# Kernel tuning notes

Hardware: AMD Instinct MI355X
Metric: run time of the kernel (lower is better)

Reference implementation:

```python
import jax, jax.numpy as jnp
import numpy as np

G = 32               # sdf grid resolution (grid_size init default)
SCALE_FACTOR = 0.2   # forward default scale_factor
EPS = 1e-12


def setup_inputs() -> dict:
    key = jax.random.key(0)
    k1, k2 = jax.random.split(key)
    H, V, F = 2, 778, 1538  # two hands, MANO topology
    vertices = jax.random.normal(k1, (H, V, 3), dtype=jnp.float32)
    faces = jax.random.randint(k2, (F, 3), 0, V, dtype=jnp.int32)
    return {"vertices": vertices, "faces": faces}


def _sdiv(n, d):
    return n / jnp.where(jnp.abs(d) < EPS, EPS, d)


def _point_tri_dist2(p, a, b, c):
    # p: [P,1,3]; a,b,c: [1,F,3] -> squared distance [P,F] (Ericson closest-point)
    ab = b - a; ac = c - a; ap = p - a
    d1 = jnp.sum(ab * ap, -1); d2 = jnp.sum(ac * ap, -1)
    bp = p - b; d3 = jnp.sum(ab * bp, -1); d4 = jnp.sum(ac * bp, -1)
    cp = p - c; d5 = jnp.sum(ab * cp, -1); d6 = jnp.sum(ac * cp, -1)
    vc = d1 * d4 - d3 * d2
    vb = d5 * d2 - d1 * d6
    va = d3 * d6 - d5 * d4
    denom = va + vb + vc
    v_in = _sdiv(vb, denom); w_in = _sdiv(vc, denom)
    res = a + ab * v_in[..., None] + ac * w_in[..., None]  # face interior
    # edge BC
    cond = ((va <= 0) & ((d4 - d3) >= 0) & ((d5 - d6) >= 0))[..., None]
    w = _sdiv(d4 - d3, (d4 - d3) + (d5 - d6))[..., None]
    res = jnp.where(cond, b + (c - b) * w, res)
    # edge AC
    cond = ((vb <= 0) & (d2 >= 0) & (d6 <= 0))[..., None]
    w = _sdiv(d2, d2 - d6)[..., None]
    res = jnp.where(cond, a + ac * w, res)
    # edge AB
    cond = ((vc <= 0) & (d1 >= 0) & (d3 <= 0))[..., None]
    w = _sdiv(d1, d1 - d3)[..., None]
    res = jnp.where(cond, a + ab * w, res)
    # vertex regions (highest precedence)
    res = jnp.where(((d6 >= 0) & (d5 <= d6))[..., None], jnp.broadcast_to(c, res.shape), res)
    res = jnp.where(((d3 >= 0) & (d4 <= d3))[..., None], jnp.broadcast_to(b, res.shape), res)
    res = jnp.where(((d1 <= 0) & (d2 <= 0))[..., None], jnp.broadcast_to(a, res.shape), res)
    return jnp.sum((p - res) ** 2, -1)


def _inside(p, a, b, c):
    # parity of +x ray intersections (Moller-Trumbore with dir = (1,0,0))
    e1 = b - a; e2 = c - a
    det = e1[..., 1] * (-e2[..., 2]) + e1[..., 2] * e2[..., 1]  # dot(e1, cross(dir,e2))
    inv = _sdiv(1.0, det)
    s = p - a
    u = (s[..., 1] * (-e2[..., 2]) + s[..., 2] * e2[..., 1]) * inv
    q = jnp.cross(s, e1)
    v = q[..., 0] * inv                # dot(dir, q)
    t = jnp.sum(e2 * q, -1) * inv
    hit = (jnp.abs(det) > 1e-9) & (u >= 0) & (u <= 1) & (v >= 0) & (u + v <= 1) & (t > 0)
    return (jnp.sum(hit.astype(jnp.int32), axis=-1) % 2) == 1


def _sdf_grid(tri):
    # tri: [F,3,3] scaled triangles -> phi [G,G,G] laid out [z,y,x] (grid_sample DHW)
    a = tri[None, :, 0]; b = tri[None, :, 1]; c = tri[None, :, 2]
    lin = jnp.linspace(-1.0, 1.0, G, dtype=tri.dtype)
    zz, yy, xx = jnp.meshgrid(lin, lin, lin, indexing='ij')
    pts = jnp.stack([xx, yy, zz], -1).reshape(G, G * G, 3)  # chunk over z-slabs

    def slab(ps):
        p = ps[:, None, :]
        d2 = jnp.min(_point_tri_dist2(p, a, b, c), axis=1)
        ins = _inside(p, a, b, c)
        return jnp.where(ins, jnp.sqrt(jnp.maximum(d2, 0.0)), 0.0)

    return jax.lax.map(slab, pts).reshape(G, G, G)


def _trilinear(phi, coords):
    # grid_sample(align_corners=True, padding_mode='zeros'), coords [N,3] in xyz order
    g = G - 1
    f = (coords + 1.0) * 0.5 * g
    fx, fy, fz = f[:, 0], f[:, 1], f[:, 2]
    x0f = jnp.floor(fx); y0f = jnp.floor(fy); z0f = jnp.floor(fz)
    wx = fx - x0f; wy = fy - y0f; wz = fz - z0f
    x0 = x0f.astype(jnp.int32); y0 = y0f.astype(jnp.int32); z0 = z0f.astype(jnp.int32)

    def corner(zi, yi, xi, w):
        valid = (zi >= 0) & (zi <= g) & (yi >= 0) & (yi <= g) & (xi >= 0) & (xi <= g)
        val = phi[jnp.clip(zi, 0, g), jnp.clip(yi, 0, g), jnp.clip(xi, 0, g)]
        return jnp.where(valid, val, 0.0) * w

    out = (corner(z0, y0, x0, (1 - wz) * (1 - wy) * (1 - wx))
           + corner(z0, y0, x0 + 1, (1 - wz) * (1 - wy) * wx)
           + corner(z0, y0 + 1, x0, (1 - wz) * wy * (1 - wx))
           + corner(z0, y0 + 1, x0 + 1, (1 - wz) * wy * wx)
           + corner(z0 + 1, y0, x0, wz * (1 - wy) * (1 - wx))
           + corner(z0 + 1, y0, x0 + 1, wz * (1 - wy) * wx)
           + corner(z0 + 1, y0 + 1, x0, wz * wy * (1 - wx))
           + corner(z0 + 1, y0 + 1, x0 + 1, wz * wy * wx))
    return out


def reference(vertices, faces):
    H = vertices.shape[0]
    bmin = vertices.min(axis=1)   # [H,3]
    bmax = vertices.max(axis=1)
    center = jax.lax.stop_gradient(((bmin + bmax) * 0.5)[:, None, :])           # [H,1,3]
    scale = jax.lax.stop_gradient(
        ((1.0 + SCALE_FACTOR) * 0.5 * (bmax - bmin).max(-1))[:, None, None])    # [H,1,1]
    v_scaled = jax.lax.stop_gradient((vertices - center) / scale)
    tris = v_scaled[:, faces]                                                    # [H,F,3,3]
    phi = jax.lax.stop_gradient(jax.vmap(_sdf_grid)(tris))                       # [H,G,G,G]
    i = 1  # hardcoded loop 'for i in [1]' in the source
    coords = ((vertices - center[i][None]) / scale[i][None]).reshape(-1, 3)
    phi_val = _trilinear(phi[i], coords).reshape(H, -1)
    weights = jnp.ones((H, 1), dtype=vertices.dtype).at[i, 0].set(0.0)
    loss = jnp.sum(weights * phi_val) / (H ** 2)
    return loss
```

## Files before the change

### kernel.cpp

```cpp
#include <hip/hip_runtime.h>
#include <math.h>

#define NNODE 32768
#define NTHR  256
#define STHR  1024
#define CH    256
#define MAXC  (CH + 63)
#define SUMB  8

__device__ __forceinline__ float rguard(float d) {
    float dd = (fabsf(d) < 1e-12f) ? 1e-12f : d;
    return __builtin_amdgcn_rcpf(dd);
}

__device__ __forceinline__ void cell_of(float px, float py, float pz,
                                        int& x0, int& y0, int& z0,
                                        float& wx, float& wy, float& wz) {
#pragma clang fp contract(off)
    float fx = (px + 1.0f) * 0.5f * 31.0f;
    float fy = (py + 1.0f) * 0.5f * 31.0f;
    float fz = (pz + 1.0f) * 0.5f * 31.0f;
    float x0f = floorf(fx), y0f = floorf(fy), z0f = floorf(fz);
    wx = fx - x0f; wy = fy - y0f; wz = fz - z0f;
    x0 = (int)fmaxf(fminf(x0f, 33.0f), -2.0f);
    y0 = (int)fmaxf(fminf(y0f, 33.0f), -2.0f);
    z0 = (int)fmaxf(fminf(z0f, 33.0f), -2.0f);
}

__device__ __forceinline__ void bbox_of(const float* __restrict__ verts, int V,
                                        float& ocx, float& ocy, float& ocz,
                                        float& osc) {
#pragma clang fp contract(off)
    const float* v1 = verts + (size_t)V * 3;
    float mn[3] = {1e30f, 1e30f, 1e30f};
    float mx[3] = {-1e30f, -1e30f, -1e30f};
    for (int i = threadIdx.x; i < V; i += blockDim.x) {
        for (int c = 0; c < 3; ++c) {
            float val = v1[i * 3 + c];
            mn[c] = fminf(mn[c], val);
            mx[c] = fmaxf(mx[c], val);
        }
    }
    for (int off = 32; off >= 1; off >>= 1) {
        for (int c = 0; c < 3; ++c) {
            mn[c] = fminf(mn[c], __shfl_down(mn[c], off));
            mx[c] = fmaxf(mx[c], __shfl_down(mx[c], off));
        }
    }
    __shared__ float smn[16][3], smx[16][3];
    int wv = threadIdx.x >> 6, lane = threadIdx.x & 63;
    if (lane == 0)
        for (int c = 0; c < 3; ++c) { smn[wv][c] = mn[c]; smx[wv][c] = mx[c]; }
    __syncthreads();
    const int nw = (int)blockDim.x >> 6;
    float ext = -1e30f, cc[3];
    for (int c = 0; c < 3; ++c) {
        float lo = 1e30f, hi = -1e30f;
        for (int w = 0; w < nw; ++w) {
            lo = fminf(lo, smn[w][c]);
            hi = fmaxf(hi, smx[w][c]);
        }
        cc[c] = (lo + hi) * 0.5f;
        ext = fmaxf(ext, hi - lo);
    }
    ocx = cc[0]; ocy = cc[1]; ocz = cc[2];
    osc = (1.0f + 0.2f) * 0.5f * ext;
    __syncthreads();
}

__device__ __forceinline__ void tri_node(
        float ax, float ay, float az, float abx, float aby, float abz,
        float acx, float acy, float acz, float inv, float det,
        float dbb, float dbc, float dcc,
        float px, float py, float pz, float& mind2, int& h) {
    float apx = px - ax, apy = py - ay, apz = pz - az;
    {
#pragma clang fp contract(fast)
        float d1 = abx * apx + aby * apy + abz * apz;
        float d2 = acx * apx + acy * apy + acz * apz;
        float d3 = d1 - dbb;
        float d4 = d2 - dbc;
        float d5 = d1 - dbc;
        float d6 = d2 - dcc;
        float vc = d1 * d4 - d3 * d2;
        float vb = d5 * d2 - d1 * d6;
        float va = d3 * d6 - d5 * d4;
        float denom = va + vb + vc;
        float rd = rguard(denom);
        float v_in = vb * rd, w_in = vc * rd;
        float rx = ax + abx * v_in + acx * w_in;
        float ry = ay + aby * v_in + acy * w_in;
        float rz = az + abz * v_in + acz * w_in;
        if (va <= 0.0f && (d4 - d3) >= 0.0f && (d5 - d6) >= 0.0f) {
            float w2 = (d4 - d3) * rguard((d4 - d3) + (d5 - d6));
            rx = ax + abx + (acx - abx) * w2;
            ry = ay + aby + (acy - aby) * w2;
            rz = az + abz + (acz - abz) * w2;
        }
        if (vb <= 0.0f && d2 >= 0.0f && d6 <= 0.0f) {
            float w2 = d2 * rguard(d2 - d6);
            rx = ax + acx * w2; ry = ay + acy * w2; rz = az + acz * w2;
        }
        if (vc <= 0.0f && d1 >= 0.0f && d3 <= 0.0f) {
            float w2 = d1 * rguard(d1 - d3);
            rx = ax + abx * w2; ry = ay + aby * w2; rz = az + abz * w2;
        }
        if (d6 >= 0.0f && d5 <= d6) { rx = ax + acx; ry = ay + acy; rz = az + acz; }
        if (d3 >= 0.0f && d4 <= d3) { rx = ax + abx; ry = ay + aby; rz = az + abz; }
        if (d1 <= 0.0f && d2 <= 0.0f) { rx = ax; ry = ay; rz = az; }
        float ddx = px - rx, ddy = py - ry, ddz = pz - rz;
        mind2 = fminf(mind2, ddx * ddx + ddy * ddy + ddz * ddz);
    }
    {
#pragma clang fp contract(off)
        float u = (apy * (-acz) + apz * acy) * inv;
        float qx = apy * abz - apz * aby;
        float qy = apz * abx - apx * abz;
        float qz = apx * aby - apy * abx;
        float v = qx * inv;
        float tt = (acx * qx + acy * qy + acz * qz) * inv;
        h += (fabsf(det) > 1e-9f && u >= 0.0f && u <= 1.0f && v >= 0.0f &&
              (u + v) <= 1.0f && tt > 0.0f) ? 1 : 0;
    }
}

__global__ void __launch_bounds__(STHR) k_setup(
        const float* __restrict__ verts, const int* __restrict__ faces,
        float* __restrict__ tri, unsigned int* __restrict__ d2b,
        int* __restrict__ hits, int* __restrict__ cnt,
        unsigned long long* __restrict__ acc, int* __restrict__ done2,
        int* __restrict__ list, int V, int F) {
    float cx0, cy0, cz0, sc;
    bbox_of(verts, V, cx0, cy0, cz0, sc);
    const int b = (int)blockIdx.x, tid = threadIdx.x;

    if (b == 0) {
        __shared__ unsigned bm[NNODE / 32];
        __shared__ int scnt[STHR];
        bm[tid] = 0u;
        __syncthreads();
        for (int i = tid; i < V; i += STHR) {
#pragma clang fp contract(off)
            float px = (verts[i * 3 + 0] - cx0) / sc;
            float py = (verts[i * 3 + 1] - cy0) / sc;
            float pz = (verts[i * 3 + 2] - cz0) / sc;
            int x0, y0, z0; float wx, wy, wz;
            cell_of(px, py, pz, x0, y0, z0, wx, wy, wz);
            for (int k = 0; k < 8; ++k) {
                int zi = z0 + ((k >> 2) & 1), yi = y0 + ((k >> 1) & 1),
                    xi = x0 + (k & 1);
                if ((unsigned)zi < 32u && (unsigned)yi < 32u && (unsigned)xi < 32u) {
                    int node = (zi * 32 + yi) * 32 + xi;
                    atomicOr(&bm[node >> 5], 1u << (node & 31));
                }
            }
        }
        __syncthreads();
        unsigned w0 = bm[tid];
        int c = __popc(w0);
        scnt[tid] = c;
        __syncthreads();
        for (int off = 1; off < STHR; off <<= 1) {
            int v_ = (tid >= off) ? scnt[tid - off] : 0;
            __syncthreads();
            scnt[tid] += v_;
            __syncthreads();
        }
        int total = scnt[STHR - 1];
        if (tid == STHR - 1) cnt[0] = total;
        int off = scnt[tid] - c;
        int basebit = tid * 32;
        while (w0) {
            int bb = __ffs(w0) - 1;
            list[off++] = basebit + bb;
            w0 &= w0 - 1;
        }
        __syncthreads();
        for (int t = tid; t < total; t += STHR) {
            int nd = list[t];
            d2b[nd] = 0xFFFFFFFFu;
            hits[nd] = 0;
        }
        if (tid == 0) { acc[0] = 0ull; done2[0] = 0; }
    } else {
        int f = (b - 1) * STHR + tid;
        if (f < F) {
#pragma clang fp contract(off)
            const float* v1 = verts + (size_t)V * 3;
            int i0 = faces[f * 3 + 0], i1 = faces[f * 3 + 1], i2 = faces[f * 3 + 2];
            float ax = (v1[i0 * 3 + 0] - cx0) / sc, ay = (v1[i0 * 3 + 1] - cy0) / sc,
                  az = (v1[i0 * 3 + 2] - cz0) / sc;
            float bx = (v1[i1 * 3 + 0] - cx0) / sc, by = (v1[i1 * 3 + 1] - cy0) / sc,
                  bz = (v1[i1 * 3 + 2] - cz0) / sc;
            float cx = (v1[i2 * 3 + 0] - cx0) / sc, cy = (v1[i2 * 3 + 1] - cy0) / sc,
                  cz = (v1[i2 * 3 + 2] - cz0) / sc;
            float abx = bx - ax, aby = by - ay, abz = bz - az;
            float acx = cx - ax, acy = cy - ay, acz = cz - az;
            float det = aby * (-acz) + abz * acy;
            float dd = (fabsf(det) < 1e-12f) ? 1e-12f : det;
            float inv = 1.0f / dd;
            float* r = tri + (size_t)f * 16;
            r[0] = ax;  r[1] = ay;  r[2] = az;
            r[3] = abx; r[4] = aby; r[5] = abz;
            r[6] = acx; r[7] = acy; r[8] = acz;
            r[9] = inv; r[10] = det;
            r[11] = abx * abx + aby * aby + abz * abz;
            r[12] = abx * acx + aby * acy + abz * acz;
            r[13] = acx * acx + acy * acy + acz * acz;
            r[14] = 0.0f; r[15] = 0.0f;
        }
    }
}

__global__ void __launch_bounds__(NTHR) k_main(
        const float* __restrict__ tri, const int* __restrict__ list,
        const int* __restrict__ cnt, unsigned int* __restrict__ d2b,
        int* __restrict__ hits, int F, int nch) {
    const int n = cnt[0];
    const int group = (int)blockIdx.x / nch;
    if (group * 4 >= n) return;
    const int c = (int)blockIdx.x - group * nch;
    const int cbase = c * CH;
    const int tn = (c == nch - 1) ? (F - cbase) : CH;

    __shared__ float s[14][MAXC];
    const int tid = threadIdx.x, lane = tid & 63;
    for (int j = tid; j < tn; j += NTHR) {
        const float4* g = (const float4*)(tri + (size_t)(cbase + j) * 16);
        float4 r0 = g[0], r1 = g[1], r2 = g[2], r3 = g[3];
        s[0][j] = r0.x;  s[1][j] = r0.y;  s[2][j] = r0.z;  s[3][j] = r0.w;
        s[4][j] = r1.x;  s[5][j] = r1.y;  s[6][j] = r1.z;  s[7][j] = r1.w;
        s[8][j] = r2.x;  s[9][j] = r2.y;  s[10][j] = r2.z; s[11][j] = r2.w;
        s[12][j] = r3.x; s[13][j] = r3.y;
    }
    __syncthreads();

    const int idx = group * 4 + (tid >> 6);
    const int node = (idx < n) ? list[idx] : -1;
    float px = 0, py = 0, pz = 0;
    if (node >= 0) {
#pragma clang fp contract(off)
        px = (float)((double)(node & 31) * (2.0 / 31.0) - 1.0);
        py = (float)((double)((node >> 5) & 31) * (2.0 / 31.0) - 1.0);
        pz = (float)((double)(node >> 10) * (2.0 / 31.0) - 1.0);
    }
    float m = 1e30f;
    int h = 0;
    if (node >= 0) {
        for (int mi = 0; mi * 64 < tn; ++mi) {
            int j = lane + mi * 64;
            if (j < tn) {
                tri_node(s[0][j], s[1][j], s[2][j], s[3][j], s[4][j], s[5][j],
                         s[6][j], s[7][j], s[8][j], s[9][j], s[10][j],
                         s[11][j], s[12][j], s[13][j], px, py, pz, m, h);
            }
        }
    }
    for (int off = 32; off >= 1; off >>= 1) {
        m = fminf(m, __shfl_xor(m, off));
        h += __shfl_xor(h, off);
    }
    if (lane == 0 && node >= 0) {
        atomicMin(d2b + node, __float_as_uint(m));
        atomicAdd(hits + node, h);
    }
}

__global__ void __launch_bounds__(NTHR) k_sum(
        const float* __restrict__ verts, const unsigned int* __restrict__ d2b,
        const int* __restrict__ hits, unsigned long long* __restrict__ acc,
        int* __restrict__ done2, float* __restrict__ out, int V) {
    float cx, cy, cz, sc;
    bbox_of(verts, V, cx, cy, cz, sc);
    float val = 0.0f;
    {
#pragma clang fp contract(off)
        for (int i = (int)blockIdx.x * NTHR + threadIdx.x; i < V; i += SUMB * NTHR) {
            float px = (verts[i * 3 + 0] - cx) / sc;
            float py = (verts[i * 3 + 1] - cy) / sc;
            float pz = (verts[i * 3 + 2] - cz) / sc;
            int x0, y0, z0; float wx, wy, wz;
            cell_of(px, py, pz, x0, y0, z0, wx, wy, wz);
            auto corner = [&](int zi, int yi, int xi, float w) -> float {
#pragma clang fp contract(off)
                bool valid = (zi >= 0) && (zi <= 31) && (yi >= 0) && (yi <= 31) &&
                             (xi >= 0) && (xi <= 31);
                int zc = min(max(zi, 0), 31);
                int yc = min(max(yi, 0), 31);
                int xc = min(max(xi, 0), 31);
                int idx = (zc * 32 + yc) * 32 + xc;
                float vv = (hits[idx] & 1)
                               ? sqrtf(fmaxf(__uint_as_float(d2b[idx]), 0.0f))
                               : 0.0f;
                return valid ? vv * w : 0.0f;
            };
            val += corner(z0, y0, x0, (1.0f - wz) * (1.0f - wy) * (1.0f - wx))
                 + corner(z0, y0, x0 + 1, (1.0f - wz) * (1.0f - wy) * wx)
                 + corner(z0, y0 + 1, x0, (1.0f - wz) * wy * (1.0f - wx))
                 + corner(z0, y0 + 1, x0 + 1, (1.0f - wz) * wy * wx)
                 + corner(z0 + 1, y0, x0, wz * (1.0f - wy) * (1.0f - wx))
                 + corner(z0 + 1, y0, x0 + 1, wz * (1.0f - wy) * wx)
                 + corner(z0 + 1, y0 + 1, x0, wz * wy * (1.0f - wx))
                 + corner(z0 + 1, y0 + 1, x0 + 1, wz * wy * wx);
        }
    }
    __shared__ float sm[NTHR];
    const int tid = threadIdx.x;
    sm[tid] = val;
    __syncthreads();
    for (int ss = NTHR / 2; ss >= 1; ss >>= 1) {
        if (tid < ss) sm[tid] += sm[tid + ss];
        __syncthreads();
    }
    if (tid == 0) {
        unsigned long long fx =
            (unsigned long long)((double)sm[0] * 4294967296.0);
        atomicAdd(acc, fx);
        asm volatile("s_waitcnt vmcnt(0)");
        int prev = atomicAdd(done2, 1);
        if (prev == SUMB - 1) {
            unsigned long long tot = atomicAdd(acc, 0ull);
            out[0] = (float)((double)tot / 4294967296.0 * 0.25);
        }
    }
}

extern "C" void kernel_launch(void* const* d_in, const int* in_sizes, int n_in,
                              void* d_out, int out_size, void* d_ws, size_t ws_size,
                              hipStream_t stream) {
    const float* verts = (const float*)d_in[0];
    const int* faces = (const int*)d_in[1];
    float* out = (float*)d_out;
    float* ws = (float*)d_ws;

    int V = in_sizes[0] / 6;
    int F = in_sizes[1] / 3;

    unsigned long long* acc = (unsigned long long*)ws;
    int* done2 = (int*)(ws + 2);
    int* cnt = (int*)(ws + 3);
    float* tri = ws + 4;
    unsigned int* d2b = (unsigned int*)(tri + 16 * (size_t)F);
    int* hits = (int*)(d2b + NNODE);
    int* list = hits + NNODE;

    int nch = F / CH;
    int rem = F - nch * CH;
    if (nch == 0 || rem >= 64) nch += (rem > 0 ? 1 : 0);
    if (nch == 0) nch = 1;

    int nrec = (F + STHR - 1) / STHR;
    int nmax = 8 * V; if (nmax > NNODE) nmax = NNODE;
    int nblk_main = ((nmax + 3) / 4) * nch;

    k_setup<<<1 + nrec, STHR, 0, stream>>>(verts, faces, tri, d2b, hits, cnt, acc,
                                           done2, list, V, F);
    k_main<<<nblk_main, NTHR, 0, stream>>>(tri, list, cnt, d2b, hits, F, nch);
    k_sum<<<SUMB, NTHR, 0, stream>>>(verts, d2b, hits, acc, done2, out, V);
}
```

Baseline: 44.34 us.

## Fuse SDF grid and sum kernels with persistent grid and hierarchical arrival barrier

Merges the per-node distance kernel and the trilinear sum kernel into one persistent kernel with a fixed grid of 2048 blocks that grid-stride over (node group, triangle chunk) work items. A two-level atomic arrival counter designates the last eight finishing cohorts as a crew. The crew spin-waits until every cohort has arrived, then reads the grid through relaxed agent-scope atomic loads and does the final reduction. This removes one kernel launch and the launch gap between stages. In exchange it adds a spin barrier that relies on all crew blocks being resident at once, plus grid-stride loop overhead.

```diff
diff --git a/kernel.cpp b/kernel.cpp
--- a/kernel.cpp
+++ b/kernel.cpp
@@ -6,7 +6,9 @@
 #define STHR  1024
 #define CH    256
 #define MAXC  (CH + 63)
-#define SUMB  8
+#define FGRID 2048
+#define NL1   64
+#define CREW  8
 
 __device__ __forceinline__ float rguard(float d) {
     float dd = (fabsf(d) < 1e-12f) ? 1e-12f : d;
@@ -129,6 +131,7 @@
         float* __restrict__ tri, unsigned int* __restrict__ d2b,
         int* __restrict__ hits, int* __restrict__ cnt,
         unsigned long long* __restrict__ acc, int* __restrict__ done2,
+        int* __restrict__ lvl1, int* __restrict__ lvl2,
         int* __restrict__ list, int V, int F) {
     float cx0, cy0, cz0, sc;
     bbox_of(verts, V, cx0, cy0, cz0, sc);
@@ -181,7 +184,8 @@
             d2b[nd] = 0xFFFFFFFFu;
             hits[nd] = 0;
         }
-        if (tid == 0) { acc[0] = 0ull; done2[0] = 0; }
+        if (tid < NL1) lvl1[tid * 16] = 0;
+        if (tid == 0) { acc[0] = 0ull; done2[0] = 0; lvl2[0] = 0; }
     } else {
         int f = (b - 1) * STHR + tid;
         if (f < F) {
@@ -212,70 +216,94 @@
     }
 }
 
-__global__ void __launch_bounds__(NTHR) k_main(
+__global__ void __launch_bounds__(NTHR) k_fused(
         const float* __restrict__ tri, const int* __restrict__ list,
         const int* __restrict__ cnt, unsigned int* __restrict__ d2b,
-        int* __restrict__ hits, int F, int nch) {
+        int* __restrict__ hits, int* __restrict__ lvl1, int* __restrict__ lvl2,
+        unsigned long long* __restrict__ acc, int* __restrict__ done2,
+        const float* __restrict__ verts, float* __restrict__ out,
+        int F, int nch, int V) {
     const int n = cnt[0];
-    const int group = (int)blockIdx.x / nch;
-    if (group * 4 >= n) return;
-    const int c = (int)blockIdx.x - group * nch;
-    const int cbase = c * CH;
-    const int tn = (c == nch - 1) ? (F - cbase) : CH;
-
+    const int ngroups = (n + 3) >> 2;
+    const int total = ngroups * nch;
+    const int tid = threadIdx.x, lane = tid & 63;
     __shared__ float s[14][MAXC];
-    const int tid = threadIdx.x, lane = tid & 63;
-    for (int j = tid; j < tn; j += NTHR) {
-        const float4* g = (const float4*)(tri + (size_t)(cbase + j) * 16);
-        float4 r0 = g[0], r1 = g[1], r2 = g[2], r3 = g[3];
-        s[0][j] = r0.x;  s[1][j] = r0.y;  s[2][j] = r0.z;  s[3][j] = r0.w;
-        s[4][j] = r1.x;  s[5][j] = r1.y;  s[6][j] = r1.z;  s[7][j] = r1.w;
-        s[8][j] = r2.x;  s[9][j] = r2.y;  s[10][j] = r2.z; s[11][j] = r2.w;
-        s[12][j] = r3.x; s[13][j] = r3.y;
-    }
-    __syncthreads();
-
-    const int idx = group * 4 + (tid >> 6);
-    const int node = (idx < n) ? list[idx] : -1;
-    float px = 0, py = 0, pz = 0;
-    if (node >= 0) {
-#pragma clang fp contract(off)
-        px = (float)((double)(node & 31) * (2.0 / 31.0) - 1.0);
-        py = (float)((double)((node >> 5) & 31) * (2.0 / 31.0) - 1.0);
-        pz = (float)((double)(node >> 10) * (2.0 / 31.0) - 1.0);
-    }
-    float m = 1e30f;
-    int h = 0;
-    if (node >= 0) {
-        for (int mi = 0; mi * 64 < tn; ++mi) {
-            int j = lane + mi * 64;
-            if (j < tn) {
-                tri_node(s[0][j], s[1][j], s[2][j], s[3][j], s[4][j], s[5][j],
-                         s[6][j], s[7][j], s[8][j], s[9][j], s[10][j],
-                         s[11][j], s[12][j], s[13][j], px, py, pz, m, h);
+
+    for (int item = (int)blockIdx.x; item < total; item += FGRID) {
+        const int group = item / nch;
+        const int c = item - group * nch;
+        const int cbase = c * CH;
+        const int tn = (c == nch - 1) ? (F - cbase) : CH;
+
+        for (int j = tid; j < tn; j += NTHR) {
+            const float4* g = (const float4*)(tri + (size_t)(cbase + j) * 16);
+            float4 r0 = g[0], r1 = g[1], r2 = g[2], r3 = g[3];
+            s[0][j] = r0.x;  s[1][j] = r0.y;  s[2][j] = r0.z;  s[3][j] = r0.w;
+            s[4][j] = r1.x;  s[5][j] = r1.y;  s[6][j] = r1.z;  s[7][j] = r1.w;
+            s[8][j] = r2.x;  s[9][j] = r2.y;  s[10][j] = r2.z; s[11][j] = r2.w;
+            s[12][j] = r3.x; s[13][j] = r3.y;
+        }
+        __syncthreads();
+
+        const int idx = group * 4 + (tid >> 6);
+        const int node = (idx < n) ? list[idx] : -1;
+        float px = 0, py = 0, pz = 0;
+        if (node >= 0) {
+#pragma clang fp contract(off)
+            px = (float)((double)(node & 31) * (2.0 / 31.0) - 1.0);
+            py = (float)((double)((node >> 5) & 31) * (2.0 / 31.0) - 1.0);
+            pz = (float)((double)(node >> 10) * (2.0 / 31.0) - 1.0);
+        }
+        float m = 1e30f;
+        int h = 0;
+        if (node >= 0) {
+            for (int mi = 0; mi * 64 < tn; ++mi) {
+                int j = lane + mi * 64;
+                if (j < tn) {
+                    tri_node(s[0][j], s[1][j], s[2][j], s[3][j], s[4][j], s[5][j],
+                             s[6][j], s[7][j], s[8][j], s[9][j], s[10][j],
+                             s[11][j], s[12][j], s[13][j], px, py, pz, m, h);
+                }
             }
         }
-    }
-    for (int off = 32; off >= 1; off >>= 1) {
-        m = fminf(m, __shfl_xor(m, off));
-        h += __shfl_xor(h, off);
-    }
-    if (lane == 0 && node >= 0) {
-        atomicMin(d2b + node, __float_as_uint(m));
-        atomicAdd(hits + node, h);
-    }
-}
-
-__global__ void __launch_bounds__(NTHR) k_sum(
-        const float* __restrict__ verts, const unsigned int* __restrict__ d2b,
-        const int* __restrict__ hits, unsigned long long* __restrict__ acc,
-        int* __restrict__ done2, float* __restrict__ out, int V) {
+        for (int off = 32; off >= 1; off >>= 1) {
+            m = fminf(m, __shfl_xor(m, off));
+            h += __shfl_xor(h, off);
+        }
+        if (lane == 0 && node >= 0) {
+            atomicMin(d2b + node, __float_as_uint(m));
+            atomicAdd(hits + node, h);
+        }
+        __syncthreads();
+    }
+
+    __shared__ int crew_slice;
+    __syncthreads();
+    if (tid == 0) {
+        crew_slice = -1;
+        int cohort = (int)blockIdx.x & (NL1 - 1);
+        int quota = (FGRID + NL1 - 1 - cohort) / NL1;
+        int p1 = atomicAdd(&lvl1[cohort * 16], 1);
+        if (p1 == quota - 1) {
+            int p2 = atomicAdd(lvl2, 1);
+            if (p2 >= NL1 - CREW) {
+                while (__hip_atomic_load(lvl2, __ATOMIC_RELAXED,
+                                         __HIP_MEMORY_SCOPE_AGENT) < NL1)
+                    __builtin_amdgcn_s_sleep(1);
+                crew_slice = p2 - (NL1 - CREW);
+            }
+        }
+    }
+    __syncthreads();
+    const int slice = crew_slice;
+    if (slice < 0) return;
+
     float cx, cy, cz, sc;
     bbox_of(verts, V, cx, cy, cz, sc);
     float val = 0.0f;
     {
 #pragma clang fp contract(off)
-        for (int i = (int)blockIdx.x * NTHR + threadIdx.x; i < V; i += SUMB * NTHR) {
+        for (int i = slice * NTHR + tid; i < V; i += CREW * NTHR) {
             float px = (verts[i * 3 + 0] - cx) / sc;
             float py = (verts[i * 3 + 1] - cy) / sc;
             float pz = (verts[i * 3 + 2] - cz) / sc;
@@ -289,9 +317,12 @@
                 int yc = min(max(yi, 0), 31);
                 int xc = min(max(xi, 0), 31);
                 int idx = (zc * 32 + yc) * 32 + xc;
-                float vv = (hits[idx] & 1)
-                               ? sqrtf(fmaxf(__uint_as_float(d2b[idx]), 0.0f))
-                               : 0.0f;
+                unsigned dbits = __hip_atomic_load(&d2b[idx], __ATOMIC_RELAXED,
+                                                   __HIP_MEMORY_SCOPE_AGENT);
+                int hh = __hip_atomic_load(&hits[idx], __ATOMIC_RELAXED,
+                                           __HIP_MEMORY_SCOPE_AGENT);
+                float vv = (hh & 1) ? sqrtf(fmaxf(__uint_as_float(dbits), 0.0f))
+                                    : 0.0f;
                 return valid ? vv * w : 0.0f;
             };
             val += corner(z0, y0, x0, (1.0f - wz) * (1.0f - wy) * (1.0f - wx))
@@ -305,7 +336,6 @@
         }
     }
     __shared__ float sm[NTHR];
-    const int tid = threadIdx.x;
     sm[tid] = val;
     __syncthreads();
     for (int ss = NTHR / 2; ss >= 1; ss >>= 1) {
@@ -318,7 +348,7 @@
         atomicAdd(acc, fx);
         asm volatile("s_waitcnt vmcnt(0)");
         int prev = atomicAdd(done2, 1);
-        if (prev == SUMB - 1) {
+        if (prev == CREW - 1) {
             unsigned long long tot = atomicAdd(acc, 0ull);
             out[0] = (float)((double)tot / 4294967296.0 * 0.25);
         }
@@ -339,7 +369,9 @@
     unsigned long long* acc = (unsigned long long*)ws;
     int* done2 = (int*)(ws + 2);
     int* cnt = (int*)(ws + 3);
-    float* tri = ws + 4;
+    int* lvl2 = (int*)(ws + 4);
+    int* lvl1 = (int*)(ws + 16);
+    float* tri = ws + 16 + NL1 * 16;
     unsigned int* d2b = (unsigned int*)(tri + 16 * (size_t)F);
     int* hits = (int*)(d2b + NNODE);
     int* list = hits + NNODE;
@@ -350,11 +382,9 @@
     if (nch == 0) nch = 1;
 
     int nrec = (F + STHR - 1) / STHR;
-    int nmax = 8 * V; if (nmax > NNODE) nmax = NNODE;
-    int nblk_main = ((nmax + 3) / 4) * nch;
 
     k_setup<<<1 + nrec, STHR, 0, stream>>>(verts, faces, tri, d2b, hits, cnt, acc,
-                                           done2, list, V, F);
-    k_main<<<nblk_main, NTHR, 0, stream>>>(tri, list, cnt, d2b, hits, F, nch);
-    k_sum<<<SUMB, NTHR, 0, stream>>>(verts, d2b, hits, acc, done2, out, V);
-}
+                                           done2, lvl1, lvl2, list, V, F);
+    k_fused<<<FGRID, NTHR, 0, stream>>>(tri, list, cnt, d2b, hits, lvl1, lvl2, acc,
+                                        done2, verts, out, F, nch, V);
+}
```

New measurement: 43.99 us. Within noise of the previous version (-0.8%).
